# Kernel tuning notes

Hardware: AMD Instinct MI355X
Metric: run time of the kernel (lower is better)

Reference implementation:

```python
import jax, jax.numpy as jnp
import numpy as np

NUM_EXPERTS = 8
AUX_LOSS_COEF = 0.01


def setup_inputs() -> dict:
    key = jax.random.key(0)
    ks = jax.random.split(key, 5)
    B, S, D, E, H = 4, 2048, 1024, NUM_EXPERTS, 4096
    scale = 0.02  # typical init scale so gelu/softmax stay in sane ranges
    return {
        "hidden_states": jax.random.normal(ks[0], (B, S, D), dtype=jnp.float32),
        "router_w": jax.random.normal(ks[1], (D, E), dtype=jnp.float32) * scale,
        "router_b": jnp.zeros((E,), dtype=jnp.float32),
        "w1": jax.random.normal(ks[2], (E, D, H), dtype=jnp.float32) * scale,
        "b1": jnp.zeros((E, H), dtype=jnp.float32),
        "w2": jax.random.normal(ks[3], (E, H, D), dtype=jnp.float32) * scale,
        "b2": jnp.zeros((E, D), dtype=jnp.float32),
    }


def reference(hidden_states, router_w, router_b, w1, b1, w2, b2):
    B, S, D = hidden_states.shape
    E = w1.shape[0]
    x = hidden_states.reshape(-1, D)  # [T, D] flattened tokens

    # Switch router: top-1 expert, combine weight = softmax prob of chosen expert
    logits = x @ router_w + router_b                      # [T, E]
    probs = jax.nn.softmax(logits, axis=-1)               # [T, E]
    sel = jnp.argmax(logits, axis=-1)                     # [T] int
    gate = jnp.take_along_axis(probs, sel[:, None], axis=1)[:, 0]  # [T]

    # Expert FFNs: per-expert Linear -> gelu -> Linear, masked top-1 combine.
    # Loop is over the small fixed expert count (structurally distinct weights).
    out = jnp.zeros_like(x)
    for e in range(E):
        h = jax.nn.gelu(x @ w1[e] + b1[e])                # [T, H]
        ye = h @ w2[e] + b2[e]                            # [T, D]
        mask = (sel == e).astype(x.dtype)
        out = out + (mask * gate)[:, None] * ye

    # Switch load-balancing auxiliary loss
    mean_probs = probs.mean(axis=0)                       # [E]
    assignments = jnp.mean(jax.nn.one_hot(sel, E, dtype=x.dtype), axis=0)  # [E]
    aux_loss = jnp.sum(mean_probs * assignments) * E
    total_loss = AUX_LOSS_COEF * aux_loss

    return out.reshape(B, S, D), total_loss
```

## Files before the change

### kernel.cpp

```cpp
#include <hip/hip_runtime.h>
#include <cstdint>

typedef __bf16 bf16_t;
typedef __attribute__((ext_vector_type(8))) __bf16 bf16x8;
typedef __attribute__((ext_vector_type(4))) float f32x4;
typedef unsigned short ushort_t;

#define TOKENS 8192
#define DIM 1024
#define HID 4096
#define NEXP 8

__device__ __forceinline__ void gl_lds16(const void* g, void* l) {
  __builtin_amdgcn_global_load_lds(
      (__attribute__((address_space(1))) void*)(void*)g,
      (__attribute__((address_space(3))) void*)l, 16, 0, 0);
}

__device__ __forceinline__ float gelu_tanh(float x) {
  float z = 0.7978845608028654f * (x + 0.044715f * x * x * x);
  z = fminf(fmaxf(z, -15.f), 15.f);
  float e = __expf(-2.f * z);
  float th = (1.f - e) / (1.f + e);
  return 0.5f * x * (1.f + th);
}

__global__ void router_kernel(const float* __restrict__ x, const float* __restrict__ rw,
                              const float* __restrict__ rbias, bf16_t* __restrict__ xb,
                              int* __restrict__ sel, float* __restrict__ gate,
                              float* __restrict__ pprob, int* __restrict__ pcnt) {
  __shared__ float sprob[NEXP];
  __shared__ int scnt[NEXP];
  int t = threadIdx.x, lane = t & 63, wave = t >> 6;
  if (t < NEXP) { sprob[t] = 0.f; scnt[t] = 0; }
  __syncthreads();
  int tok = blockIdx.x * 4 + wave;
  const float* xp = x + (size_t)tok * DIM + lane * 16;
  float acc[NEXP];
#pragma unroll
  for (int e = 0; e < NEXP; ++e) acc[e] = 0.f;
  ushort_t xv[16];
#pragma unroll
  for (int j = 0; j < 16; j += 4) {
    float4 v = *(const float4*)(xp + j);
    const float* wr = rw + (size_t)(lane * 16 + j) * NEXP;
    float c[4] = {v.x, v.y, v.z, v.w};
#pragma unroll
    for (int d = 0; d < 4; ++d) {
      xv[j + d] = __builtin_bit_cast(ushort_t, (bf16_t)c[d]);
#pragma unroll
      for (int e = 0; e < NEXP; ++e) acc[e] += c[d] * wr[d * NEXP + e];
    }
  }
  {
    uint4* xop = (uint4*)(xb + (size_t)tok * DIM + lane * 16);
    xop[0] = ((uint4*)xv)[0];
    xop[1] = ((uint4*)xv)[1];
  }
#pragma unroll
  for (int s = 1; s < 64; s <<= 1)
#pragma unroll
    for (int e = 0; e < NEXP; ++e) acc[e] += __shfl_xor(acc[e], s);
  if (lane == 0) {
    float lg[NEXP];
#pragma unroll
    for (int e = 0; e < NEXP; ++e) lg[e] = acc[e] + rbias[e];
    float mx = lg[0]; int am = 0;
#pragma unroll
    for (int e = 1; e < NEXP; ++e) if (lg[e] > mx) { mx = lg[e]; am = e; }
    float p[NEXP]; float se = 0.f;
#pragma unroll
    for (int e = 0; e < NEXP; ++e) { p[e] = __expf(lg[e] - mx); se += p[e]; }
    float inv = 1.f / se;
#pragma unroll
    for (int e = 0; e < NEXP; ++e) { p[e] *= inv; atomicAdd(&sprob[e], p[e]); }
    sel[tok] = am;
    gate[tok] = p[am];
    atomicAdd(&scnt[am], 1);
  }
  __syncthreads();
  if (t < NEXP) {
    pprob[blockIdx.x * NEXP + t] = sprob[t];
    pcnt[blockIdx.x * NEXP + t] = scnt[t];
  }
}

__global__ void tcvt2_kernel(const float* __restrict__ w1, const float* __restrict__ w2,
                             bf16_t* __restrict__ w1t, bf16_t* __restrict__ w2t) {
  __shared__ float tile[64][65];
  int y = blockIdx.y;
  int which = y >> 3, e = y & 7;
  int R = which ? HID : DIM;
  int C = which ? DIM : HID;
  const float* src = (which ? w2 : w1) + (size_t)e * R * C;
  bf16_t* dst = (which ? w2t : w1t) + (size_t)e * R * C;
  int cbt = C >> 6;
  int rt = blockIdx.x / cbt, ct = blockIdx.x % cbt;
  int rb = rt * 64, cb = ct * 64;
  int t = threadIdx.x;
  int r = t >> 2, cq = (t & 3) * 16;
  const float* sp = src + (size_t)(rb + r) * C + cb + cq;
#pragma unroll
  for (int j = 0; j < 16; j += 4) {
    float4 v = *(const float4*)(sp + j);
    tile[r][cq + j + 0] = v.x; tile[r][cq + j + 1] = v.y;
    tile[r][cq + j + 2] = v.z; tile[r][cq + j + 3] = v.w;
  }
  __syncthreads();
  int oc = t >> 2, orr = (t & 3) * 16;
  ushort_t tmp[16];
#pragma unroll
  for (int j = 0; j < 16; ++j) {
    bf16_t b = (bf16_t)tile[orr + j][oc];
    tmp[j] = __builtin_bit_cast(ushort_t, b);
  }
  uint4* dp = (uint4*)(dst + (size_t)(cb + oc) * R + rb + orr);
  dp[0] = ((uint4*)tmp)[0];
  dp[1] = ((uint4*)tmp)[1];
}

__global__ void reduce_kernel(const float* __restrict__ pprob, const int* __restrict__ pcnt,
                              int nb, int* __restrict__ counts, int* __restrict__ offsets,
                              int* __restrict__ cursors, float* __restrict__ loss_out) {
  __shared__ float fred[256];
  __shared__ int ired[256];
  int t = threadIdx.x;
  int e = t & 7, i0 = t >> 3;
  float fs = 0.f; int is = 0;
  for (int i = i0; i < nb; i += 32) { fs += pprob[i * 8 + e]; is += pcnt[i * 8 + e]; }
  fred[t] = fs; ired[t] = is;
  __syncthreads();
  if (t < NEXP) {
    float tp = 0.f; int tc = 0;
    for (int j = 0; j < 32; ++j) { tp += fred[j * 8 + t]; tc += ired[j * 8 + t]; }
    counts[t] = tc;
    fred[t] = tp;
    cursors[t] = 0;
  }
  __syncthreads();
  if (t == 0) {
    int off = 0; float loss = 0.f;
    for (int q = 0; q < NEXP; ++q) {
      offsets[q] = off; off += counts[q];
      loss += (fred[q] / (float)TOKENS) * ((float)counts[q] / (float)TOKENS);
    }
    *loss_out = loss * (float)NEXP * 0.01f;
  }
}

__global__ void scatter_kernel(const int* __restrict__ sel, const int* __restrict__ offsets,
                               int* __restrict__ cursors, int* __restrict__ idxl) {
  int tok = blockIdx.x * 256 + threadIdx.x;
  int lane = threadIdx.x & 63;
  int e = sel[tok];
#pragma unroll
  for (int ex = 0; ex < NEXP; ++ex) {
    unsigned long long mask = __ballot(e == ex);
    if (e == ex) {
      int leader = __ffsll(mask) - 1;
      int total = __popcll(mask);
      int rank = __popcll(mask & ((1ull << lane) - 1ull));
      int base = 0;
      if (lane == leader) base = atomicAdd(&cursors[ex], total);
      base = __shfl(base, leader);
      idxl[offsets[ex] + base + rank] = tok;
    }
  }
}

__global__ __launch_bounds__(256) void gemm1_kernel(
    const bf16_t* __restrict__ xb, const bf16_t* __restrict__ w1t,
    const float* __restrict__ b1, const int* __restrict__ idxl,
    const int* __restrict__ counts, const int* __restrict__ offsets,
    bf16_t* __restrict__ h) {
  int e = blockIdx.z;
  int cnt = counts[e];
  int f = blockIdx.y * 32 + blockIdx.x;
  int lf = (f & 7) * 256 + (f >> 3);
  int mt = lf & 63, nt = lf >> 6;
  int mBase = mt * 128;
  if (mBase >= cnt) return;
  int nBase = nt * 128;
  int off = offsets[e];
  __shared__ bf16_t As[4096], Bs[4096];
  int t = threadIdx.x, lane = t & 63, wave = t >> 6;
  int wrow = wave >> 1, wcol = wave & 1;
  f32x4 acc[4][4];
#pragma unroll
  for (int m = 0; m < 4; ++m)
#pragma unroll
    for (int n = 0; n < 4; ++n) acc[m][n] = (f32x4){0.f, 0.f, 0.f, 0.f};

  int srow = wave * 16 + (lane >> 2);
  int kin = (lane & 3) * 8;
  int c1 = cnt - 1;
  int slot0 = mBase + srow; slot0 = slot0 < c1 ? slot0 : c1;
  int slot1 = mBase + srow + 64; slot1 = slot1 < c1 ? slot1 : c1;
  int tok0 = idxl[off + slot0], tok1 = idxl[off + slot1];
  const bf16_t* ag0 = xb + (size_t)tok0 * DIM + kin;
  const bf16_t* ag1 = xb + (size_t)tok1 * DIM + kin;
  const bf16_t* wb = w1t + (size_t)e * HID * DIM;
  const bf16_t* bg0 = wb + (size_t)(nBase + srow) * DIM + kin;
  const bf16_t* bg1 = bg0 + (size_t)64 * DIM;
  bf16_t* lA0 = As + wave * 512;
  bf16_t* lA1 = As + 2048 + wave * 512;
  bf16_t* lB0 = Bs + wave * 512;
  bf16_t* lB1 = Bs + 2048 + wave * 512;
  int kcol = (lane >> 4) * 8;

  for (int kt = 0; kt < DIM / 32; ++kt) {
    int k0 = kt * 32;
    gl_lds16(ag0 + k0, lA0);
    gl_lds16(ag1 + k0, lA1);
    gl_lds16(bg0 + k0, lB0);
    gl_lds16(bg1 + k0, lB1);
    __syncthreads();
    bf16x8 af[4], bv[4];
#pragma unroll
    for (int m = 0; m < 4; ++m)
      af[m] = *(const bf16x8*)(As + (wrow * 64 + m * 16 + (lane & 15)) * 32 + kcol);
#pragma unroll
    for (int n = 0; n < 4; ++n)
      bv[n] = *(const bf16x8*)(Bs + (wcol * 64 + n * 16 + (lane & 15)) * 32 + kcol);
#pragma unroll
    for (int m = 0; m < 4; ++m)
#pragma unroll
      for (int n = 0; n < 4; ++n)
        acc[m][n] = __builtin_amdgcn_mfma_f32_16x16x32_bf16(af[m], bv[n], acc[m][n], 0, 0, 0);
    __syncthreads();
  }

  float bias[4];
#pragma unroll
  for (int n = 0; n < 4; ++n) bias[n] = b1[e * HID + nBase + wcol * 64 + n * 16 + (lane & 15)];
#pragma unroll
  for (int m = 0; m < 4; ++m) {
    int rb0 = mBase + wrow * 64 + m * 16 + (lane >> 4) * 4;
#pragma unroll
    for (int j = 0; j < 4; ++j) {
      int r = rb0 + j;
      if (r < cnt) {
        bf16_t* hp = h + (size_t)(off + r) * HID + nBase + wcol * 64 + (lane & 15);
#pragma unroll
        for (int n = 0; n < 4; ++n)
          hp[n * 16] = (bf16_t)gelu_tanh(acc[m][n][j] + bias[n]);
      }
    }
  }
}

__global__ __launch_bounds__(512) void gemm2_kernel(
    const bf16_t* __restrict__ h, const bf16_t* __restrict__ w2t,
    const float* __restrict__ b2, const int* __restrict__ idxl,
    const float* __restrict__ gate, const int* __restrict__ counts,
    const int* __restrict__ offsets, float* __restrict__ out) {
  int e = blockIdx.z;
  int cnt = counts[e];
  int f = blockIdx.y * 8 + blockIdx.x;
  int lf = (f & 7) * 64 + (f >> 3);
  int mt = lf & 63, nt = lf >> 6;
  int mBase = mt * 128;
  if (mBase >= cnt) return;
  int nBase = nt * 128;
  int off = offsets[e];
  __shared__ bf16_t S[8192];
  int t = threadIdx.x, lane = t & 63, wave = t >> 6;
  int wrow = wave >> 2, wcol = wave & 3;
  f32x4 acc[4][2];
#pragma unroll
  for (int m = 0; m < 4; ++m)
#pragma unroll
    for (int n = 0; n < 2; ++n) acc[m][n] = (f32x4){0.f, 0.f, 0.f, 0.f};

  int srow = wave * 16 + (lane >> 2);
  int kin = (lane & 3) * 8;
  int c1 = cnt - 1;
  int slot = mBase + srow; slot = slot < c1 ? slot : c1;
  const bf16_t* agA = h + (size_t)(off + slot) * HID + kin;
  const bf16_t* agB = w2t + (size_t)e * DIM * HID + (size_t)(nBase + srow) * HID + kin;
  bf16_t* lA = S + wave * 512;
  bf16_t* lB = S + 4096 + wave * 512;
  int kcol = (lane >> 4) * 8;

  for (int kt = 0; kt < HID / 32; ++kt) {
    int k0 = kt * 32;
    gl_lds16(agA + k0, lA);
    gl_lds16(agB + k0, lB);
    __syncthreads();
    bf16x8 af[4], bv[2];
#pragma unroll
    for (int m = 0; m < 4; ++m)
      af[m] = *(const bf16x8*)(S + (wrow * 64 + m * 16 + (lane & 15)) * 32 + kcol);
#pragma unroll
    for (int n = 0; n < 2; ++n)
      bv[n] = *(const bf16x8*)(S + 4096 + (wcol * 32 + n * 16 + (lane & 15)) * 32 + kcol);
#pragma unroll
    for (int m = 0; m < 4; ++m)
#pragma unroll
      for (int n = 0; n < 2; ++n)
        acc[m][n] = __builtin_amdgcn_mfma_f32_16x16x32_bf16(af[m], bv[n], acc[m][n], 0, 0, 0);
    __syncthreads();
  }

  float bias[2];
#pragma unroll
  for (int n = 0; n < 2; ++n) bias[n] = b2[e * DIM + nBase + wcol * 32 + n * 16 + (lane & 15)];
#pragma unroll
  for (int m = 0; m < 4; ++m) {
    int rb0 = mBase + wrow * 64 + m * 16 + (lane >> 4) * 4;
#pragma unroll
    for (int j = 0; j < 4; ++j) {
      int r = rb0 + j;
      if (r < cnt) {
        int tok = idxl[off + r];
        float g = gate[tok];
        float* op = out + (size_t)tok * DIM + nBase + wcol * 32 + (lane & 15);
#pragma unroll
        for (int n = 0; n < 2; ++n)
          op[n * 16] = g * (acc[m][n][j] + bias[n]);
      }
    }
  }
}

extern "C" void kernel_launch(void* const* d_in, const int* in_sizes, int n_in,
                              void* d_out, int out_size, void* d_ws, size_t ws_size,
                              hipStream_t stream) {
  const float* hs = (const float*)d_in[0];
  const float* rw = (const float*)d_in[1];
  const float* rb = (const float*)d_in[2];
  const float* w1 = (const float*)d_in[3];
  const float* b1 = (const float*)d_in[4];
  const float* w2 = (const float*)d_in[5];
  const float* b2 = (const float*)d_in[6];
  float* out = (float*)d_out;
  char* ws = (char*)d_ws;

  bf16_t* xb   = (bf16_t*)(ws + 0);
  bf16_t* w1t  = (bf16_t*)(ws + 16777216);
  bf16_t* w2t  = (bf16_t*)(ws + 83886080);
  bf16_t* hbuf = (bf16_t*)(ws + 150994944);
  int*   sel   = (int*)  (ws + 219152384);
  float* gate  = (float*)(ws + 219185152);
  int*   idxl  = (int*)  (ws + 219217920);
  float* pprob = (float*)(ws + 219250688);
  int*   pcnt  = (int*)  (ws + 219316224);
  int*   counts  = (int*)(ws + 219381760);
  int*   offsets = counts + 8;
  int*   cursors = counts + 16;

  router_kernel<<<2048, 256, 0, stream>>>(hs, rw, rb, xb, sel, gate, pprob, pcnt);
  tcvt2_kernel<<<dim3(1024, 16), 256, 0, stream>>>(w1, w2, w1t, w2t);
  reduce_kernel<<<1, 256, 0, stream>>>(pprob, pcnt, 2048, counts, offsets, cursors,
                                       out + (out_size - 1));
  scatter_kernel<<<32, 256, 0, stream>>>(sel, offsets, cursors, idxl);
  gemm1_kernel<<<dim3(32, 64, 8), 256, 0, stream>>>(xb, w1t, b1, idxl, counts, offsets, hbuf);
  gemm2_kernel<<<dim3(8, 64, 8), 512, 0, stream>>>(hbuf, w2t, b2, idxl, gate, counts, offsets, out);
}
```

Before: 409.4 us.

## Double-buffer LDS tiles in both expert GEMMs to overlap loads with MFMA

Both GEMM kernels now keep two LDS buffers for the A and B tiles. The loads for the next k-tile are issued before computing on the current one, and there is one barrier per iteration instead of two. The goal is to hide global-to-LDS latency behind matrix math. It doubles LDS use per block, which may reduce occupancy. Correctness depends on the single barrier covering completion of the async global_load_lds writes, because no explicit vmcnt wait is added.

```diff
diff --git a/kernel.cpp b/kernel.cpp
--- a/kernel.cpp
+++ b/kernel.cpp
@@ -182,7 +182,7 @@
   if (mBase >= cnt) return;
   int nBase = nt * 128;
   int off = offsets[e];
-  __shared__ bf16_t As[4096], Bs[4096];
+  __shared__ bf16_t As[2][4096], Bs[2][4096];
   int t = threadIdx.x, lane = t & 63, wave = t >> 6;
   int wrow = wave >> 1, wcol = wave & 1;
   f32x4 acc[4][4];
@@ -202,32 +202,57 @@
   const bf16_t* wb = w1t + (size_t)e * HID * DIM;
   const bf16_t* bg0 = wb + (size_t)(nBase + srow) * DIM + kin;
   const bf16_t* bg1 = bg0 + (size_t)64 * DIM;
-  bf16_t* lA0 = As + wave * 512;
-  bf16_t* lA1 = As + 2048 + wave * 512;
-  bf16_t* lB0 = Bs + wave * 512;
-  bf16_t* lB1 = Bs + 2048 + wave * 512;
+  int ldoff = wave * 512;
   int kcol = (lane >> 4) * 8;
 
-  for (int kt = 0; kt < DIM / 32; ++kt) {
-    int k0 = kt * 32;
-    gl_lds16(ag0 + k0, lA0);
-    gl_lds16(ag1 + k0, lA1);
-    gl_lds16(bg0 + k0, lB0);
-    gl_lds16(bg1 + k0, lB1);
+  gl_lds16(ag0, As[0] + ldoff);
+  gl_lds16(ag1, As[0] + 2048 + ldoff);
+  gl_lds16(bg0, Bs[0] + ldoff);
+  gl_lds16(bg1, Bs[0] + 2048 + ldoff);
+  __syncthreads();
+
+  int cur = 0;
+  for (int kt = 0; kt < DIM / 32 - 1; ++kt) {
+    int nxt = cur ^ 1;
+    int k1 = (kt + 1) * 32;
+    gl_lds16(ag0 + k1, As[nxt] + ldoff);
+    gl_lds16(ag1 + k1, As[nxt] + 2048 + ldoff);
+    gl_lds16(bg0 + k1, Bs[nxt] + ldoff);
+    gl_lds16(bg1 + k1, Bs[nxt] + 2048 + ldoff);
+    {
+      const bf16_t* Ac = As[cur];
+      const bf16_t* Bc = Bs[cur];
+      bf16x8 af[4], bv[4];
+#pragma unroll
+      for (int m = 0; m < 4; ++m)
+        af[m] = *(const bf16x8*)(Ac + (wrow * 64 + m * 16 + (lane & 15)) * 32 + kcol);
+#pragma unroll
+      for (int n = 0; n < 4; ++n)
+        bv[n] = *(const bf16x8*)(Bc + (wcol * 64 + n * 16 + (lane & 15)) * 32 + kcol);
+#pragma unroll
+      for (int m = 0; m < 4; ++m)
+#pragma unroll
+        for (int n = 0; n < 4; ++n)
+          acc[m][n] = __builtin_amdgcn_mfma_f32_16x16x32_bf16(af[m], bv[n], acc[m][n], 0, 0, 0);
+    }
     __syncthreads();
+    cur = nxt;
+  }
+  {
+    const bf16_t* Ac = As[cur];
+    const bf16_t* Bc = Bs[cur];
     bf16x8 af[4], bv[4];
 #pragma unroll
     for (int m = 0; m < 4; ++m)
-      af[m] = *(const bf16x8*)(As + (wrow * 64 + m * 16 + (lane & 15)) * 32 + kcol);
+      af[m] = *(const bf16x8*)(Ac + (wrow * 64 + m * 16 + (lane & 15)) * 32 + kcol);
 #pragma unroll
     for (int n = 0; n < 4; ++n)
-      bv[n] = *(const bf16x8*)(Bs + (wcol * 64 + n * 16 + (lane & 15)) * 32 + kcol);
+      bv[n] = *(const bf16x8*)(Bc + (wcol * 64 + n * 16 + (lane & 15)) * 32 + kcol);
 #pragma unroll
     for (int m = 0; m < 4; ++m)
 #pragma unroll
       for (int n = 0; n < 4; ++n)
         acc[m][n] = __builtin_amdgcn_mfma_f32_16x16x32_bf16(af[m], bv[n], acc[m][n], 0, 0, 0);
-    __syncthreads();
   }
 
   float bias[4];
@@ -263,7 +288,7 @@
   if (mBase >= cnt) return;
   int nBase = nt * 128;
   int off = offsets[e];
-  __shared__ bf16_t S[8192];
+  __shared__ bf16_t As[2][4096], Bs[2][4096];
   int t = threadIdx.x, lane = t & 63, wave = t >> 6;
   int wrow = wave >> 2, wcol = wave & 3;
   f32x4 acc[4][2];
@@ -278,28 +303,53 @@
   int slot = mBase + srow; slot = slot < c1 ? slot : c1;
   const bf16_t* agA = h + (size_t)(off + slot) * HID + kin;
   const bf16_t* agB = w2t + (size_t)e * DIM * HID + (size_t)(nBase + srow) * HID + kin;
-  bf16_t* lA = S + wave * 512;
-  bf16_t* lB = S + 4096 + wave * 512;
+  int ldoff = wave * 512;
   int kcol = (lane >> 4) * 8;
 
-  for (int kt = 0; kt < HID / 32; ++kt) {
-    int k0 = kt * 32;
-    gl_lds16(agA + k0, lA);
-    gl_lds16(agB + k0, lB);
+  gl_lds16(agA, As[0] + ldoff);
+  gl_lds16(agB, Bs[0] + ldoff);
+  __syncthreads();
+
+  int cur = 0;
+  for (int kt = 0; kt < HID / 32 - 1; ++kt) {
+    int nxt = cur ^ 1;
+    int k1 = (kt + 1) * 32;
+    gl_lds16(agA + k1, As[nxt] + ldoff);
+    gl_lds16(agB + k1, Bs[nxt] + ldoff);
+    {
+      const bf16_t* Ac = As[cur];
+      const bf16_t* Bc = Bs[cur];
+      bf16x8 af[4], bv[2];
+#pragma unroll
+      for (int m = 0; m < 4; ++m)
+        af[m] = *(const bf16x8*)(Ac + (wrow * 64 + m * 16 + (lane & 15)) * 32 + kcol);
+#pragma unroll
+      for (int n = 0; n < 2; ++n)
+        bv[n] = *(const bf16x8*)(Bc + (wcol * 32 + n * 16 + (lane & 15)) * 32 + kcol);
+#pragma unroll
+      for (int m = 0; m < 4; ++m)
+#pragma unroll
+        for (int n = 0; n < 2; ++n)
+          acc[m][n] = __builtin_amdgcn_mfma_f32_16x16x32_bf16(af[m], bv[n], acc[m][n], 0, 0, 0);
+    }
     __syncthreads();
+    cur = nxt;
+  }
+  {
+    const bf16_t* Ac = As[cur];
+    const bf16_t* Bc = Bs[cur];
     bf16x8 af[4], bv[2];
 #pragma unroll
     for (int m = 0; m < 4; ++m)
-      af[m] = *(const bf16x8*)(S + (wrow * 64 + m * 16 + (lane & 15)) * 32 + kcol);
+      af[m] = *(const bf16x8*)(Ac + (wrow * 64 + m * 16 + (lane & 15)) * 32 + kcol);
 #pragma unroll
     for (int n = 0; n < 2; ++n)
-      bv[n] = *(const bf16x8*)(S + 4096 + (wcol * 32 + n * 16 + (lane & 15)) * 32 + kcol);
+      bv[n] = *(const bf16x8*)(Bc + (wcol * 32 + n * 16 + (lane & 15)) * 32 + kcol);
 #pragma unroll
     for (int m = 0; m < 4; ++m)
 #pragma unroll
       for (int n = 0; n < 2; ++n)
         acc[m][n] = __builtin_amdgcn_mfma_f32_16x16x32_bf16(af[m], bv[n], acc[m][n], 0, 0, 0);
-    __syncthreads();
   }
 
   float bias[2];
```

Measured after the change: 417.6 us. +2.0%, slower.

## Double-buffer LDS in expert GEMMs, compact tile scheduling, cheaper GELU

Applied to the files above, without the earlier changes.

Both expert GEMMs now use two LDS buffers so the next K-tile's global-to-LDS loads are issued before computing on the current tile, overlapping memory and MFMA work. The reduce kernel builds a compact list of (expert, m-tile) pairs, so the GEMM grids launch only the needed tiles instead of a large grid of mostly early-exiting blocks. GELU tanh is rewritten as x*sigmoid form using exp and a hardware reciprocal. This doubles LDS usage per block, which may lower occupancy, and drops the previous block-order swizzle for cache locality.

```diff
diff --git a/kernel.cpp b/kernel.cpp
--- a/kernel.cpp
+++ b/kernel.cpp
@@ -11,18 +11,18 @@
 #define HID 4096
 #define NEXP 8
 
+
 __device__ __forceinline__ void gl_lds16(const void* g, void* l) {
   __builtin_amdgcn_global_load_lds(
       (__attribute__((address_space(1))) void*)(void*)g,
       (__attribute__((address_space(3))) void*)l, 16, 0, 0);
 }
 
-__device__ __forceinline__ float gelu_tanh(float x) {
-  float z = 0.7978845608028654f * (x + 0.044715f * x * x * x);
-  z = fminf(fmaxf(z, -15.f), 15.f);
-  float e = __expf(-2.f * z);
-  float th = (1.f - e) / (1.f + e);
-  return 0.5f * x * (1.f + th);
+__device__ __forceinline__ float gelu_fast(float x) {
+  float x2 = x * x;
+  float z2 = x * (1.59576912f + 0.07135482f * x2);
+  float e = __expf(-z2);
+  return x * __builtin_amdgcn_rcpf(1.f + e);
 }
 
 __global__ void router_kernel(const float* __restrict__ x, const float* __restrict__ rw,
@@ -120,8 +120,7 @@
 }
 
 __global__ void reduce_kernel(const float* __restrict__ pprob, const int* __restrict__ pcnt,
-                              int nb, int* __restrict__ counts, int* __restrict__ offsets,
-                              int* __restrict__ cursors, float* __restrict__ loss_out) {
+                              int nb, int* __restrict__ meta, float* __restrict__ loss_out) {
   __shared__ float fred[256];
   __shared__ int ired[256];
   int t = threadIdx.x;
@@ -133,26 +132,33 @@
   if (t < NEXP) {
     float tp = 0.f; int tc = 0;
     for (int j = 0; j < 32; ++j) { tp += fred[j * 8 + t]; tc += ired[j * 8 + t]; }
-    counts[t] = tc;
+    meta[t] = tc;
     fred[t] = tp;
-    cursors[t] = 0;
+    meta[16 + t] = 0;
   }
   __syncthreads();
   if (t == 0) {
-    int off = 0; float loss = 0.f;
+    int off = 0; float loss = 0.f; int s = 0;
     for (int q = 0; q < NEXP; ++q) {
-      offsets[q] = off; off += counts[q];
-      loss += (fred[q] / (float)TOKENS) * ((float)counts[q] / (float)TOKENS);
-    }
+      int c = meta[q];
+      meta[8 + q] = off;
+      int ntile = (c + 127) >> 7;
+      for (int m = 0; m < ntile; ++m) meta[32 + s++] = (q << 16) | m;
+      off += c;
+      loss += (fred[q] / (float)TOKENS) * ((float)c / (float)TOKENS);
+    }
+    meta[24] = s;
     *loss_out = loss * (float)NEXP * 0.01f;
   }
 }
 
-__global__ void scatter_kernel(const int* __restrict__ sel, const int* __restrict__ offsets,
-                               int* __restrict__ cursors, int* __restrict__ idxl) {
+__global__ void scatter_kernel(const int* __restrict__ sel, int* __restrict__ meta,
+                               int* __restrict__ idxl) {
   int tok = blockIdx.x * 256 + threadIdx.x;
   int lane = threadIdx.x & 63;
   int e = sel[tok];
+  const int* offsets = meta + 8;
+  int* cursors = meta + 16;
 #pragma unroll
   for (int ex = 0; ex < NEXP; ++ex) {
     unsigned long long mask = __ballot(e == ex);
@@ -168,22 +174,44 @@
   }
 }
 
+#define G1_STAGE(Ab, Bb, KT) do {                       \
+    int k0_ = (KT) * 32;                                \
+    gl_lds16(ag0 + k0_, Ab + ldoff);                    \
+    gl_lds16(ag1 + k0_, Ab + 2048 + ldoff);             \
+    gl_lds16(bg0 + k0_, Bb + ldoff);                    \
+    gl_lds16(bg1 + k0_, Bb + 2048 + ldoff);             \
+  } while (0)
+
+#define G1_COMP(Ab, Bb) do {                                                        \
+    bf16x8 af[4], bv[4];                                                            \
+    _Pragma("unroll")                                                               \
+    for (int m = 0; m < 4; ++m)                                                     \
+      af[m] = *(const bf16x8*)(Ab + (wrow * 64 + m * 16 + l15) * 32 + kcol);        \
+    _Pragma("unroll")                                                               \
+    for (int n = 0; n < 4; ++n)                                                     \
+      bv[n] = *(const bf16x8*)(Bb + (wcol * 64 + n * 16 + l15) * 32 + kcol);        \
+    _Pragma("unroll")                                                               \
+    for (int m = 0; m < 4; ++m)                                                     \
+      _Pragma("unroll")                                                             \
+      for (int n = 0; n < 4; ++n)                                                   \
+        acc[m][n] = __builtin_amdgcn_mfma_f32_16x16x32_bf16(af[m], bv[n], acc[m][n], 0, 0, 0); \
+  } while (0)
+
 __global__ __launch_bounds__(256) void gemm1_kernel(
     const bf16_t* __restrict__ xb, const bf16_t* __restrict__ w1t,
     const float* __restrict__ b1, const int* __restrict__ idxl,
-    const int* __restrict__ counts, const int* __restrict__ offsets,
-    bf16_t* __restrict__ h) {
-  int e = blockIdx.z;
-  int cnt = counts[e];
-  int f = blockIdx.y * 32 + blockIdx.x;
-  int lf = (f & 7) * 256 + (f >> 3);
-  int mt = lf & 63, nt = lf >> 6;
+    const int* __restrict__ meta, bf16_t* __restrict__ h) {
+  int slot = blockIdx.x;
+  if (slot >= meta[24]) return;
+  int tm = meta[32 + slot];
+  int e = tm >> 16, mt = tm & 0xffff;
+  int cnt = meta[e];
+  int off = meta[8 + e];
   int mBase = mt * 128;
-  if (mBase >= cnt) return;
-  int nBase = nt * 128;
-  int off = offsets[e];
-  __shared__ bf16_t As[4096], Bs[4096];
+  int nBase = blockIdx.y * 128;
+  __shared__ bf16_t A0[4096], A1[4096], B0[4096], B1[4096];
   int t = threadIdx.x, lane = t & 63, wave = t >> 6;
+  int l15 = lane & 15;
   int wrow = wave >> 1, wcol = wave & 1;
   f32x4 acc[4][4];
 #pragma unroll
@@ -202,37 +230,28 @@
   const bf16_t* wb = w1t + (size_t)e * HID * DIM;
   const bf16_t* bg0 = wb + (size_t)(nBase + srow) * DIM + kin;
   const bf16_t* bg1 = bg0 + (size_t)64 * DIM;
-  bf16_t* lA0 = As + wave * 512;
-  bf16_t* lA1 = As + 2048 + wave * 512;
-  bf16_t* lB0 = Bs + wave * 512;
-  bf16_t* lB1 = Bs + 2048 + wave * 512;
+  int ldoff = wave * 512;
   int kcol = (lane >> 4) * 8;
 
-  for (int kt = 0; kt < DIM / 32; ++kt) {
-    int k0 = kt * 32;
-    gl_lds16(ag0 + k0, lA0);
-    gl_lds16(ag1 + k0, lA1);
-    gl_lds16(bg0 + k0, lB0);
-    gl_lds16(bg1 + k0, lB1);
+  G1_STAGE(A0, B0, 0);
+  __syncthreads();
+#pragma unroll 1
+  for (int kt = 0; kt < DIM / 32 - 2; kt += 2) {
+    G1_STAGE(A1, B1, kt + 1);
+    G1_COMP(A0, B0);
     __syncthreads();
-    bf16x8 af[4], bv[4];
-#pragma unroll
-    for (int m = 0; m < 4; ++m)
-      af[m] = *(const bf16x8*)(As + (wrow * 64 + m * 16 + (lane & 15)) * 32 + kcol);
-#pragma unroll
-    for (int n = 0; n < 4; ++n)
-      bv[n] = *(const bf16x8*)(Bs + (wcol * 64 + n * 16 + (lane & 15)) * 32 + kcol);
-#pragma unroll
-    for (int m = 0; m < 4; ++m)
-#pragma unroll
-      for (int n = 0; n < 4; ++n)
-        acc[m][n] = __builtin_amdgcn_mfma_f32_16x16x32_bf16(af[m], bv[n], acc[m][n], 0, 0, 0);
+    G1_STAGE(A0, B0, kt + 2);
+    G1_COMP(A1, B1);
     __syncthreads();
   }
+  G1_STAGE(A1, B1, DIM / 32 - 1);
+  G1_COMP(A0, B0);
+  __syncthreads();
+  G1_COMP(A1, B1);
 
   float bias[4];
 #pragma unroll
-  for (int n = 0; n < 4; ++n) bias[n] = b1[e * HID + nBase + wcol * 64 + n * 16 + (lane & 15)];
+  for (int n = 0; n < 4; ++n) bias[n] = b1[e * HID + nBase + wcol * 64 + n * 16 + l15];
 #pragma unroll
   for (int m = 0; m < 4; ++m) {
     int rb0 = mBase + wrow * 64 + m * 16 + (lane >> 4) * 4;
@@ -240,31 +259,52 @@
     for (int j = 0; j < 4; ++j) {
       int r = rb0 + j;
       if (r < cnt) {
-        bf16_t* hp = h + (size_t)(off + r) * HID + nBase + wcol * 64 + (lane & 15);
+        bf16_t* hp = h + (size_t)(off + r) * HID + nBase + wcol * 64 + l15;
 #pragma unroll
         for (int n = 0; n < 4; ++n)
-          hp[n * 16] = (bf16_t)gelu_tanh(acc[m][n][j] + bias[n]);
+          hp[n * 16] = (bf16_t)gelu_fast(acc[m][n][j] + bias[n]);
       }
     }
   }
 }
+
+#define G2_STAGE(Ab, Bb, KT) do {                       \
+    int k0_ = (KT) * 32;                                \
+    gl_lds16(agA + k0_, Ab + ldoff);                    \
+    gl_lds16(agB + k0_, Bb + ldoff);                    \
+  } while (0)
+
+#define G2_COMP(Ab, Bb) do {                                                        \
+    bf16x8 af[4], bv[2];                                                            \
+    _Pragma("unroll")                                                               \
+    for (int m = 0; m < 4; ++m)                                                     \
+      af[m] = *(const bf16x8*)(Ab + (wrow * 64 + m * 16 + l15) * 32 + kcol);        \
+    _Pragma("unroll")                                                               \
+    for (int n = 0; n < 2; ++n)                                                     \
+      bv[n] = *(const bf16x8*)(Bb + (wcol * 32 + n * 16 + l15) * 32 + kcol);        \
+    _Pragma("unroll")                                                               \
+    for (int m = 0; m < 4; ++m)                                                     \
+      _Pragma("unroll")                                                             \
+      for (int n = 0; n < 2; ++n)                                                   \
+        acc[m][n] = __builtin_amdgcn_mfma_f32_16x16x32_bf16(af[m], bv[n], acc[m][n], 0, 0, 0); \
+  } while (0)
 
 __global__ __launch_bounds__(512) void gemm2_kernel(
     const bf16_t* __restrict__ h, const bf16_t* __restrict__ w2t,
     const float* __restrict__ b2, const int* __restrict__ idxl,
-    const float* __restrict__ gate, const int* __restrict__ counts,
-    const int* __restrict__ offsets, float* __restrict__ out) {
-  int e = blockIdx.z;
-  int cnt = counts[e];
-  int f = blockIdx.y * 8 + blockIdx.x;
-  int lf = (f & 7) * 64 + (f >> 3);
-  int mt = lf & 63, nt = lf >> 6;
+    const float* __restrict__ gate, const int* __restrict__ meta,
+    float* __restrict__ out) {
+  int slot = blockIdx.x;
+  if (slot >= meta[24]) return;
+  int tm = meta[32 + slot];
+  int e = tm >> 16, mt = tm & 0xffff;
+  int cnt = meta[e];
+  int off = meta[8 + e];
   int mBase = mt * 128;
-  if (mBase >= cnt) return;
-  int nBase = nt * 128;
-  int off = offsets[e];
-  __shared__ bf16_t S[8192];
+  int nBase = blockIdx.y * 128;
+  __shared__ bf16_t A0[4096], A1[4096], B0[4096], B1[4096];
   int t = threadIdx.x, lane = t & 63, wave = t >> 6;
+  int l15 = lane & 15;
   int wrow = wave >> 2, wcol = wave & 3;
   f32x4 acc[4][2];
 #pragma unroll
@@ -275,36 +315,31 @@
   int srow = wave * 16 + (lane >> 2);
   int kin = (lane & 3) * 8;
   int c1 = cnt - 1;
-  int slot = mBase + srow; slot = slot < c1 ? slot : c1;
-  const bf16_t* agA = h + (size_t)(off + slot) * HID + kin;
+  int slotc = mBase + srow; slotc = slotc < c1 ? slotc : c1;
+  const bf16_t* agA = h + (size_t)(off + slotc) * HID + kin;
   const bf16_t* agB = w2t + (size_t)e * DIM * HID + (size_t)(nBase + srow) * HID + kin;
-  bf16_t* lA = S + wave * 512;
-  bf16_t* lB = S + 4096 + wave * 512;
+  int ldoff = wave * 512;
   int kcol = (lane >> 4) * 8;
 
-  for (int kt = 0; kt < HID / 32; ++kt) {
-    int k0 = kt * 32;
-    gl_lds16(agA + k0, lA);
-    gl_lds16(agB + k0, lB);
+  G2_STAGE(A0, B0, 0);
+  __syncthreads();
+#pragma unroll 1
+  for (int kt = 0; kt < HID / 32 - 2; kt += 2) {
+    G2_STAGE(A1, B1, kt + 1);
+    G2_COMP(A0, B0);
     __syncthreads();
-    bf16x8 af[4], bv[2];
-#pragma unroll
-    for (int m = 0; m < 4; ++m)
-      af[m] = *(const bf16x8*)(S + (wrow * 64 + m * 16 + (lane & 15)) * 32 + kcol);
-#pragma unroll
-    for (int n = 0; n < 2; ++n)
-      bv[n] = *(const bf16x8*)(S + 4096 + (wcol * 32 + n * 16 + (lane & 15)) * 32 + kcol);
-#pragma unroll
-    for (int m = 0; m < 4; ++m)
-#pragma unroll
-      for (int n = 0; n < 2; ++n)
-        acc[m][n] = __builtin_amdgcn_mfma_f32_16x16x32_bf16(af[m], bv[n], acc[m][n], 0, 0, 0);
+    G2_STAGE(A0, B0, kt + 2);
+    G2_COMP(A1, B1);
     __syncthreads();
   }
+  G2_STAGE(A1, B1, HID / 32 - 1);
+  G2_COMP(A0, B0);
+  __syncthreads();
+  G2_COMP(A1, B1);
 
   float bias[2];
 #pragma unroll
-  for (int n = 0; n < 2; ++n) bias[n] = b2[e * DIM + nBase + wcol * 32 + n * 16 + (lane & 15)];
+  for (int n = 0; n < 2; ++n) bias[n] = b2[e * DIM + nBase + wcol * 32 + n * 16 + l15];
 #pragma unroll
   for (int m = 0; m < 4; ++m) {
     int rb0 = mBase + wrow * 64 + m * 16 + (lane >> 4) * 4;
@@ -314,7 +349,7 @@
       if (r < cnt) {
         int tok = idxl[off + r];
         float g = gate[tok];
-        float* op = out + (size_t)tok * DIM + nBase + wcol * 32 + (lane & 15);
+        float* op = out + (size_t)tok * DIM + nBase + wcol * 32 + l15;
 #pragma unroll
         for (int n = 0; n < 2; ++n)
           op[n * 16] = g * (acc[m][n][j] + bias[n]);
@@ -345,15 +380,12 @@
   int*   idxl  = (int*)  (ws + 219217920);
   float* pprob = (float*)(ws + 219250688);
   int*   pcnt  = (int*)  (ws + 219316224);
-  int*   counts  = (int*)(ws + 219381760);
-  int*   offsets = counts + 8;
-  int*   cursors = counts + 16;
+  int*   meta  = (int*)  (ws + 219381760);
 
   router_kernel<<<2048, 256, 0, stream>>>(hs, rw, rb, xb, sel, gate, pprob, pcnt);
   tcvt2_kernel<<<dim3(1024, 16), 256, 0, stream>>>(w1, w2, w1t, w2t);
-  reduce_kernel<<<1, 256, 0, stream>>>(pprob, pcnt, 2048, counts, offsets, cursors,
-                                       out + (out_size - 1));
-  scatter_kernel<<<32, 256, 0, stream>>>(sel, offsets, cursors, idxl);
-  gemm1_kernel<<<dim3(32, 64, 8), 256, 0, stream>>>(xb, w1t, b1, idxl, counts, offsets, hbuf);
-  gemm2_kernel<<<dim3(8, 64, 8), 512, 0, stream>>>(hbuf, w2t, b2, idxl, gate, counts, offsets, out);
-}
+  reduce_kernel<<<1, 256, 0, stream>>>(pprob, pcnt, 2048, meta, out + (out_size - 1));
+  scatter_kernel<<<32, 256, 0, stream>>>(sel, meta, idxl);
+  gemm1_kernel<<<dim3(72, 32), 256, 0, stream>>>(xb, w1t, b1, idxl, meta, hbuf);
+  gemm2_kernel<<<dim3(72, 8), 512, 0, stream>>>(hbuf, w2t, b2, idxl, gate, meta, out);
+}
```

Measured after the change: 475.1 us. +16.1%, slower.
